# Performance work log

Measured on AMD Instinct MI355X. Metric: run time of the kernel, lower is better.

## Reference

```python
import jax, jax.numpy as jnp
import numpy as np

N_NODES = 30000


def gcn_conv(x, src, dst, ew, W, b, n):
    # x: [N, Fin] -> linear first (PyG GCNConv), then normalized scatter-add
    h = x @ W  # [N, Fout]
    loops = jnp.arange(n, dtype=src.dtype)
    s = jnp.concatenate([src, loops])
    d = jnp.concatenate([dst, loops])
    w = jnp.concatenate([ew, jnp.ones((n,), dtype=ew.dtype)])
    deg = jax.ops.segment_sum(w, d, num_segments=n)
    dinv = jnp.where(deg > 0, jax.lax.rsqrt(jnp.where(deg > 0, deg, 1.0)), 0.0)
    norm = dinv[s] * w * dinv[d]  # [E+N]
    msg = h[s] * norm[:, None]  # [E+N, Fout]
    out = jax.ops.segment_sum(msg, d, num_segments=n)
    return out + b


def setup_inputs() -> dict:
    key = jax.random.key(0)
    ks = jax.random.split(key, 16)
    n, e, f, c = N_NODES, 480000, 64, 64
    dims = [f, 2 * c, 4 * c, 8 * c]  # 64 -> 128 -> 256 -> 512
    num_classes = 40

    def lin(k, fi, fo):
        k1, k2 = jax.random.split(k)
        s = 1.0 / np.sqrt(fi)
        return (jax.random.uniform(k1, (fi, fo), jnp.float32, -s, s),
                jax.random.uniform(k2, (fo,), jnp.float32, -s, s))

    W1, b1 = lin(ks[0], dims[0], dims[1])
    W2, b2 = lin(ks[1], dims[1], dims[2])
    W3, b3 = lin(ks[2], dims[2], dims[3])
    fW1, fb1 = lin(ks[3], dims[3], dims[3])
    fW2, fb2 = lin(ks[4], dims[3], num_classes)
    return {
        "x": jax.random.normal(ks[5], (n, f), jnp.float32),
        "edge_index": jax.random.randint(ks[6], (2, e), 0, n, jnp.int32),
        "edge_attr": jax.random.uniform(ks[7], (e, 1), jnp.float32),
        "W1": W1, "b1": b1, "W2": W2, "b2": b2, "W3": W3, "b3": b3,
        "fW1": fW1, "fb1": fb1, "fW2": fW2, "fb2": fb2,
    }


def reference(x, edge_index, edge_attr, W1, b1, W2, b2, W3, b3, fW1, fb1, fW2, fb2):
    n = x.shape[0]
    src, dst = edge_index[0], edge_index[1]
    ew = edge_attr.squeeze(-1)
    h = jax.nn.relu(gcn_conv(x, src, dst, ew, W1, b1, n))
    h = jax.nn.relu(gcn_conv(h, src, dst, ew, W2, b2, n))
    h = jax.nn.relu(gcn_conv(h, src, dst, ew, W3, b3, n))
    h = jax.nn.relu(h @ fW1 + fb1)
    h = h @ fW2 + fb2
    return jax.nn.log_softmax(h, axis=1)
```

## Files before the change

kernel.cpp:

```cpp
#include <hip/hip_runtime.h>
#include <cstdint>
#include <cstddef>


typedef _Float16 f16;
typedef _Float16 half8 __attribute__((ext_vector_type(8)));
typedef _Float16 half4 __attribute__((ext_vector_type(4)));
typedef float v4f __attribute__((ext_vector_type(4)));
typedef unsigned long long u64;

__device__ inline void gload_lds16(const void* g, void* l) {
    __builtin_amdgcn_global_load_lds(
        (const __attribute__((address_space(1))) unsigned int*)g,
        (__attribute__((address_space(3))) unsigned int*)l, 16, 0, 0);
}


__global__ __launch_bounds__(256) void k_init(u64* packed, int n) {
    int i = blockIdx.x * blockDim.x + threadIdx.x;
    if (i < n) packed[i] = 0ULL;
}

__global__ __launch_bounds__(256) void k_edge1(const int* __restrict__ dst, const float* __restrict__ ew,
                                               u64* __restrict__ packed, int* __restrict__ eslot, int E) {
    int t = blockIdx.x * blockDim.x + threadIdx.x;
    int e0 = t * 4;
    if (e0 + 3 < E) {
        int4 d4 = *(const int4*)(dst + e0);
        float4 w4 = *(const float4*)(ew + e0);
        u64 a0 = ((u64)__float2uint_rn(w4.x * 1048576.f) << 24) | 1ULL;
        u64 a1 = ((u64)__float2uint_rn(w4.y * 1048576.f) << 24) | 1ULL;
        u64 a2 = ((u64)__float2uint_rn(w4.z * 1048576.f) << 24) | 1ULL;
        u64 a3 = ((u64)__float2uint_rn(w4.w * 1048576.f) << 24) | 1ULL;
        u64 o0 = atomicAdd(&packed[d4.x], a0);
        u64 o1 = atomicAdd(&packed[d4.y], a1);
        u64 o2 = atomicAdd(&packed[d4.z], a2);
        u64 o3 = atomicAdd(&packed[d4.w], a3);
        int4 s;
        s.x = (int)(o0 & 0xFFFFFF); s.y = (int)(o1 & 0xFFFFFF);
        s.z = (int)(o2 & 0xFFFFFF); s.w = (int)(o3 & 0xFFFFFF);
        *(int4*)(eslot + e0) = s;
    } else {
        for (int e = e0; e < E; ++e) {
            u64 a = ((u64)__float2uint_rn(ew[e] * 1048576.f) << 24) | 1ULL;
            u64 o = atomicAdd(&packed[dst[e]], a);
            eslot[e] = (int)(o & 0xFFFFFF);
        }
    }
}

__global__ __launch_bounds__(256) void k_dinv_scan1(const u64* __restrict__ packed,
                                                    float* __restrict__ dinv, int* __restrict__ cnt,
                                                    int* __restrict__ bsum, int n) {
    int i = blockIdx.x * 256 + threadIdx.x;
    int c = 0;
    if (i < n) {
        u64 pk = packed[i];
        c = (int)(pk & 0xFFFFFF);
        float d = 1.0f + (float)(pk >> 24) * (1.0f / 1048576.f);
        float r = rsqrtf(d);
        r = r * (1.5f - 0.5f * d * r * r);
        dinv[i] = r;
        cnt[i] = c;
    }
    int v = c;
#pragma unroll
    for (int o = 32; o; o >>= 1) v += __shfl_xor(v, o);
    __shared__ int s[4];
    if ((threadIdx.x & 63) == 0) s[threadIdx.x >> 6] = v;
    __syncthreads();
    if (threadIdx.x == 0) bsum[blockIdx.x] = s[0] + s[1] + s[2] + s[3];
}

__device__ inline int block_scan_incl(int v) {
    __shared__ int ws[4];
    int lane = threadIdx.x & 63, w = threadIdx.x >> 6;
#pragma unroll
    for (int off = 1; off < 64; off <<= 1) {
        int t = __shfl_up(v, off);
        if (lane >= off) v += t;
    }
    if (lane == 63) ws[w] = v;
    __syncthreads();
    int add = 0;
#pragma unroll
    for (int i = 0; i < 4; ++i) add += (i < w) ? ws[i] : 0;
    __syncthreads();
    return v + add;
}

__global__ __launch_bounds__(256) void k_scan2(const int* __restrict__ bsum, int* __restrict__ boff, int nb) {
    __shared__ int carry;
    if (threadIdx.x == 0) carry = 0;
    __syncthreads();
    for (int base = 0; base < nb; base += 256) {
        int i = base + threadIdx.x;
        int v = (i < nb) ? bsum[i] : 0;
        int incl = block_scan_incl(v);
        int c = carry;
        if (i < nb) boff[i] = c + incl - v;
        __syncthreads();
        if (threadIdx.x == 255) carry = c + incl;
        __syncthreads();
    }
}

__global__ __launch_bounds__(256) void k_scan3(const int* __restrict__ cnt, const int* __restrict__ boff,
                                               int* __restrict__ rowptr, int n) {
    int i = blockIdx.x * 256 + threadIdx.x;
    int v = (i < n) ? cnt[i] : 0;
    int incl = block_scan_incl(v);
    if (i < n) rowptr[i] = boff[blockIdx.x] + incl - v;
    if (i == n - 1) rowptr[n] = boff[blockIdx.x] + incl;
}

__global__ __launch_bounds__(256) void k_fill(const int* __restrict__ src, const int* __restrict__ dst,
                                              const float* __restrict__ ew, const int* __restrict__ eslot,
                                              const float* __restrict__ dinv, const int* __restrict__ rowptr,
                                              int* __restrict__ csr_src, float* __restrict__ csr_norm, int E) {
    int e = blockIdx.x * blockDim.x + threadIdx.x;
    if (e < E) {
        int d = dst[e], s = src[e];
        int idx = rowptr[d] + eslot[e];
        csr_src[idx] = s;
        csr_norm[idx] = dinv[s] * ew[e] * dinv[d];
    }
}

struct PrepArgs {
    const float* x; f16* xh; int xt4;
    const float* W[5]; f16* WT[5];
    int lgK[5]; int N[5]; int off[6];
};
__global__ __launch_bounds__(256) void k_prep_cast(PrepArgs a) {
    int i = blockIdx.x * 256 + threadIdx.x;
    if (i < a.xt4) {
        float4 v = *(const float4*)(a.x + (size_t)i * 4);
        half4 h = {(f16)v.x, (f16)v.y, (f16)v.z, (f16)v.w};
        *(half4*)(a.xh + (size_t)i * 4) = h;
        return;
    }
    int w = i - a.xt4;
#pragma unroll
    for (int s = 0; s < 5; ++s) {
        if (w >= a.off[s] && w < a.off[s + 1]) {
            int li = w - a.off[s];
            int K = 1 << a.lgK[s];
            int nr = li >> a.lgK[s], k = li & (K - 1);
            float v = (nr < a.N[s]) ? a.W[s][(size_t)k * a.N[s] + nr] : 0.f;
            a.WT[s][li] = (f16)v;
        }
    }
}

template <int F>
__global__ __launch_bounds__(256) void k_agg(const f16* __restrict__ h,
                                             const float* __restrict__ dinv, const int* __restrict__ rowptr,
                                             const int* __restrict__ csr_src, const float* __restrict__ csr_norm,
                                             f16* __restrict__ o, int n) {
    constexpr int LPN = F / 8;
    constexpr int NPW = 64 / LPN;
    int wave = (int)((blockIdx.x * (unsigned)blockDim.x + threadIdx.x) >> 6);
    int lane = threadIdx.x & 63;
    int grp = lane / LPN, lin = lane % LPN;
    int node = wave * NPW + grp;
    if (node >= n) return;
    float di = dinv[node], w0 = di * di;
    float acc[8];
#pragma unroll
    for (int i = 0; i < 8; ++i) acc[i] = 0.f;

    auto gat = [&](int s, float w) {
        half8 x = *(const half8*)(h + (size_t)s * F + lin * 8);
#pragma unroll
        for (int i = 0; i < 8; ++i) acc[i] += w * (float)x[i];
    };

    gat(node, w0);
    int beg = rowptr[node], end = rowptr[node + 1];
    int j = beg;
    for (; j + 3 < end; j += 4) {
        int s0 = csr_src[j], s1 = csr_src[j + 1], s2 = csr_src[j + 2], s3 = csr_src[j + 3];
        float u0 = csr_norm[j], u1 = csr_norm[j + 1], u2 = csr_norm[j + 2], u3 = csr_norm[j + 3];
        gat(s0, u0); gat(s1, u1); gat(s2, u2); gat(s3, u3);
    }
    for (; j < end; ++j) gat(csr_src[j], csr_norm[j]);

    half8 v;
#pragma unroll
    for (int i = 0; i < 8; ++i) v[i] = (f16)acc[i];
    *(half8*)(o + (size_t)node * F + (size_t)lin * 8) = v;
}

template <int WR, int WC, bool RELU, bool F16OUT>
__global__ __launch_bounds__(256) void k_mm(const f16* __restrict__ A, const f16* __restrict__ BT,
                                            const float* __restrict__ bias,
                                            f16* __restrict__ Ch, float* __restrict__ Cf,
                                            int M, int N, int K, int nB, int nwg) {
    constexpr int TM = WR * 64, TN = WC * 64;
    __shared__ f16 lsA[2][TM * 64];
    __shared__ f16 lsB[2][TN * 64];

    int wg = blockIdx.x;
    int q = nwg >> 3, r = nwg & 7;
    int xcd = wg & 7, lin = wg >> 3;
    int wgs = (xcd < r) ? (xcd * (q + 1) + lin) : (r * (q + 1) + (xcd - r) * q + lin);
    int bm = wgs / nB, bn = wgs % nB;

    int tid = threadIdx.x;
    int lane = tid & 63, wid = tid >> 6;
    int l16 = lane & 15, lhi = lane >> 4;
    int wm = (wid / WC) * 64, wn = (wid % WC) * 64;
    int brow = bm * TM, bcol = bn * TN;

    v4f acc[4][4] = {};

    auto stageA = [&](int buf, int k0) {
#pragma unroll
        for (int it = 0; it < TM / 32; ++it) {
            int b = it * 4096 + tid * 16;
            int row = b >> 7;
            int s = ((b >> 4) & 7) ^ (row & 7);
            gload_lds16(A + (size_t)(brow + row) * K + k0 + s * 8, ((char*)&lsA[buf][0]) + b);
        }
    };
    auto stageB = [&](int buf, int k0) {
#pragma unroll
        for (int it = 0; it < TN / 32; ++it) {
            int b = it * 4096 + tid * 16;
            int row = b >> 7;
            int s = ((b >> 4) & 7) ^ (row & 7);
            gload_lds16(BT + (size_t)(bcol + row) * K + k0 + s * 8, ((char*)&lsB[buf][0]) + b);
        }
    };

    int nk = K >> 6;
    stageA(0, 0);
    stageB(0, 0);
    for (int kt = 0; kt < nk; ++kt) {
        int cur = kt & 1;
        __syncthreads();
        if (kt + 1 < nk) {
            stageA(cur ^ 1, (kt + 1) << 6);
            stageB(cur ^ 1, (kt + 1) << 6);
        }
        half8 bf[2][4];
#pragma unroll
        for (int ks = 0; ks < 2; ++ks)
#pragma unroll
            for (int fn = 0; fn < 4; ++fn) {
                int row = wn + fn * 16 + l16;
                int sidx = (ks * 4 + lhi) ^ (row & 7);
                bf[ks][fn] = *(const half8*)(&lsB[cur][0] + row * 64 + sidx * 8);
            }
#pragma unroll
        for (int ks = 0; ks < 2; ++ks)
#pragma unroll
            for (int fm = 0; fm < 4; ++fm) {
                int row = wm + fm * 16 + l16;
                int sidx = (ks * 4 + lhi) ^ (row & 7);
                half8 af = *(const half8*)(&lsA[cur][0] + row * 64 + sidx * 8);
#pragma unroll
                for (int fn = 0; fn < 4; ++fn)
                    acc[fm][fn] = __builtin_amdgcn_mfma_f32_16x16x32_f16(bf[ks][fn], af, acc[fm][fn], 0, 0, 0);
            }
    }

#pragma unroll
    for (int fm = 0; fm < 4; ++fm) {
        int m = brow + wm + fm * 16 + l16;
        if (m >= M) continue;
#pragma unroll
        for (int fn = 0; fn < 4; ++fn) {
            int nb = bcol + wn + fn * 16 + lhi * 4;
            if (F16OUT) {
                v4f bv = *(const v4f*)(bias + nb);
                v4f v = acc[fm][fn] + bv;
                if (RELU) {
#pragma unroll
                    for (int rr = 0; rr < 4; ++rr) v[rr] = fmaxf(v[rr], 0.f);
                }
                half4 hv = {(f16)v[0], (f16)v[1], (f16)v[2], (f16)v[3]};
                *(half4*)(Ch + (size_t)m * N + nb) = hv;
            } else {
#pragma unroll
                for (int rr = 0; rr < 4; ++rr) {
                    int nn = nb + rr;
                    if (nn < N) {
                        float v = acc[fm][fn][rr] + bias[nn];
                        if (RELU) v = fmaxf(v, 0.f);
                        Cf[(size_t)m * N + nn] = v;
                    }
                }
            }
        }
    }
}


__device__ inline float wred_max(float v) {
#pragma unroll
    for (int o = 32; o; o >>= 1) v = fmaxf(v, __shfl_xor(v, o));
    return v;
}
__device__ inline float wred_sum(float v) {
#pragma unroll
    for (int o = 32; o; o >>= 1) v += __shfl_xor(v, o);
    return v;
}

__global__ __launch_bounds__(256) void k_lsm(const float* __restrict__ in, float* __restrict__ out, int n) {
    int gw = (int)((blockIdx.x * blockDim.x + threadIdx.x) >> 6);
    int lane = threadIdx.x & 63;
    if (gw >= n) return;
    float v = (lane < 40) ? in[(size_t)gw * 40 + lane] : -INFINITY;
    float m = wred_max(v);
    float e = (lane < 40) ? __expf(v - m) : 0.f;
    float s = wred_sum(e);
    if (lane < 40) out[(size_t)gw * 40 + lane] = v - m - __logf(s);
}


extern "C" void kernel_launch(void* const* d_in, const int* in_sizes, int n_in,
                              void* d_out, int out_size, void* d_ws, size_t ws_size,
                              hipStream_t stream) {
    const float* x   = (const float*)d_in[0];
    const int*   ei  = (const int*)d_in[1];
    const float* ea  = (const float*)d_in[2];
    const float* W1  = (const float*)d_in[3];  const float* b1  = (const float*)d_in[4];
    const float* W2  = (const float*)d_in[5];  const float* b2  = (const float*)d_in[6];
    const float* W3  = (const float*)d_in[7];  const float* b3  = (const float*)d_in[8];
    const float* fW1 = (const float*)d_in[9];  const float* fb1 = (const float*)d_in[10];
    const float* fW2 = (const float*)d_in[11]; const float* fb2 = (const float*)d_in[12];

    int n = in_sizes[0] / 64;
    int E = in_sizes[1] / 2;
    int Mpad = ((n + 255) / 256) * 256;
    const int* src = ei;
    const int* dst = ei + E;
    float* out = (float*)d_out;

    char* p = (char*)d_ws;
    auto alloc = [&](size_t bytes) -> char* {
        char* r = p;
        p += (bytes + 255) & ~(size_t)255;
        return r;
    };
    int nb256 = (n + 255) / 256;
    u64*   packed   = (u64*)alloc((size_t)n * 8);
    float* dinv     = (float*)alloc((size_t)n * 4);
    int*   cnt      = (int*)alloc((size_t)n * 4);
    int*   rowptr   = (int*)alloc((size_t)(n + 1) * 4);
    int*   bsum     = (int*)alloc((size_t)nb256 * 4);
    int*   boff     = (int*)alloc((size_t)nb256 * 4);
    int*   eslot    = (int*)alloc((size_t)E * 4);
    int*   csr_src  = (int*)alloc((size_t)E * 4);
    float* csr_norm = (float*)alloc((size_t)E * 4);
    f16* XH  = (f16*)alloc((size_t)Mpad * 64 * 2);
    f16* W1T = (f16*)alloc((size_t)128 * 64 * 2);
    f16* W2T = (f16*)alloc((size_t)256 * 128 * 2);
    f16* W3T = (f16*)alloc((size_t)512 * 256 * 2);
    f16* F1T = (f16*)alloc((size_t)512 * 512 * 2);
    f16* F2T = (f16*)alloc((size_t)128 * 512 * 2);
    f16* AGG = (f16*)alloc((size_t)Mpad * 256 * 2);
    f16* HA  = (f16*)alloc((size_t)Mpad * 512 * 2);
    f16* HB  = (f16*)alloc((size_t)Mpad * 512 * 2);
    float* logits = (float*)alloc((size_t)Mpad * 40 * 4);

    const int tb = 256;
    int nBk = (n + tb - 1) / tb;
    int eB = (E + tb - 1) / tb;
    int e4B = (E / 4 + tb - 1) / tb + 1;
    int waveB = (int)(((size_t)n * 64 + tb - 1) / tb);
    auto aggB = [&](int npw) {
        long waves = (n + npw - 1) / npw;
        return (int)((waves * 64 + tb - 1) / tb);
    };

    k_init<<<nBk, tb, 0, stream>>>(packed, n);
    k_edge1<<<e4B, tb, 0, stream>>>(dst, ea, packed, eslot, E);
    k_dinv_scan1<<<nb256, tb, 0, stream>>>(packed, dinv, cnt, bsum, n);
    k_scan2<<<1, tb, 0, stream>>>(bsum, boff, nb256);
    k_scan3<<<nb256, tb, 0, stream>>>(cnt, boff, rowptr, n);
    k_fill<<<eB, tb, 0, stream>>>(src, dst, ea, eslot, dinv, rowptr, csr_src, csr_norm, E);

    {
        PrepArgs a;
        a.x = x; a.xh = XH; a.xt4 = n * 16;
        a.W[0] = W1;  a.WT[0] = W1T; a.lgK[0] = 6; a.N[0] = 128;
        a.W[1] = W2;  a.WT[1] = W2T; a.lgK[1] = 7; a.N[1] = 256;
        a.W[2] = W3;  a.WT[2] = W3T; a.lgK[2] = 8; a.N[2] = 512;
        a.W[3] = fW1; a.WT[3] = F1T; a.lgK[3] = 9; a.N[3] = 512;
        a.W[4] = fW2; a.WT[4] = F2T; a.lgK[4] = 9; a.N[4] = 40;
        a.off[0] = 0;
        a.off[1] = a.off[0] + 128 * 64;
        a.off[2] = a.off[1] + 256 * 128;
        a.off[3] = a.off[2] + 512 * 256;
        a.off[4] = a.off[3] + 512 * 512;
        a.off[5] = a.off[4] + 128 * 512;
        int tot = a.xt4 + a.off[5];
        k_prep_cast<<<(tot + tb - 1) / tb, tb, 0, stream>>>(a);
    }

    int mB22 = Mpad / 128;
    auto mm22 = [&](const f16* a, const f16* bt, const float* bias, f16* ch, int N, int K) {
        int nB2 = N / 128;
        int nwg = mB22 * nB2;
        k_mm<2, 2, true, true><<<nwg, 256, 0, stream>>>(a, bt, bias, ch, nullptr, n, N, K, nB2, nwg);
    };

    k_agg<64><<<aggB(8), tb, 0, stream>>>(XH, dinv, rowptr, csr_src, csr_norm, AGG, n);
    mm22(AGG, W1T, b1, HA, 128, 64);
    k_agg<128><<<aggB(4), tb, 0, stream>>>(HA, dinv, rowptr, csr_src, csr_norm, AGG, n);
    mm22(AGG, W2T, b2, HB, 256, 128);
    k_agg<256><<<aggB(2), tb, 0, stream>>>(HB, dinv, rowptr, csr_src, csr_norm, AGG, n);
    mm22(AGG, W3T, b3, HA, 512, 256);
    mm22(HA, F1T, fb1, HB, 512, 512);
    {
        int nwg = Mpad / 256;
        k_mm<4, 1, false, false><<<nwg, 256, 0, stream>>>(HB, F2T, fb2, nullptr, logits, n, 40, 512, 1, nwg);
    }
    k_lsm<<<waveB, tb, 0, stream>>>(logits, out, n);
}
```

Baseline: 219.4 us.

## Fuse init into prep, add 256x256 GEMM tiles, fuse final GEMM with log-softmax

The separate zero-init kernel is folded into the prep/cast kernel, which saves one launch. The 128-wide layers (layers 2, 3 and FC1) now run a new 512-thread GEMM with 256x256 tiles, which raises data reuse and cuts the number of workgroups. The last GEMM uses a narrower B tile (64 columns, enough for 40 classes) and computes log-softmax in its epilogue, which removes the logits buffer round-trip and the separate softmax kernel. The bigger tiles use more LDS and registers, so occupancy may drop, and fewer workgroups can leave the GPU underfilled for small layers.

```diff
diff --git a/kernel.cpp b/kernel.cpp
--- a/kernel.cpp
+++ b/kernel.cpp
@@ -15,11 +15,6 @@
         (__attribute__((address_space(3))) unsigned int*)l, 16, 0, 0);
 }
 
-
-__global__ __launch_bounds__(256) void k_init(u64* packed, int n) {
-    int i = blockIdx.x * blockDim.x + threadIdx.x;
-    if (i < n) packed[i] = 0ULL;
-}
 
 __global__ __launch_bounds__(256) void k_edge1(const int* __restrict__ dst, const float* __restrict__ ew,
                                                u64* __restrict__ packed, int* __restrict__ eslot, int E) {
@@ -128,19 +123,22 @@
 }
 
 struct PrepArgs {
+    u64* packed; int n;
     const float* x; f16* xh; int xt4;
     const float* W[5]; f16* WT[5];
     int lgK[5]; int N[5]; int off[6];
 };
-__global__ __launch_bounds__(256) void k_prep_cast(PrepArgs a) {
+__global__ __launch_bounds__(256) void k_prep(PrepArgs a) {
     int i = blockIdx.x * 256 + threadIdx.x;
-    if (i < a.xt4) {
-        float4 v = *(const float4*)(a.x + (size_t)i * 4);
+    if (i < a.n) { a.packed[i] = 0ULL; return; }
+    int j = i - a.n;
+    if (j < a.xt4) {
+        float4 v = *(const float4*)(a.x + (size_t)j * 4);
         half4 h = {(f16)v.x, (f16)v.y, (f16)v.z, (f16)v.w};
-        *(half4*)(a.xh + (size_t)i * 4) = h;
+        *(half4*)(a.xh + (size_t)j * 4) = h;
         return;
     }
-    int w = i - a.xt4;
+    int w = j - a.xt4;
 #pragma unroll
     for (int s = 0; s < 5; ++s) {
         if (w >= a.off[s] && w < a.off[s + 1]) {
@@ -192,15 +190,12 @@
     *(half8*)(o + (size_t)node * F + (size_t)lin * 8) = v;
 }
 
-template <int WR, int WC, bool RELU, bool F16OUT>
+template <bool RELU>
 __global__ __launch_bounds__(256) void k_mm(const f16* __restrict__ A, const f16* __restrict__ BT,
-                                            const float* __restrict__ bias,
-                                            f16* __restrict__ Ch, float* __restrict__ Cf,
+                                            const float* __restrict__ bias, f16* __restrict__ Ch,
                                             int M, int N, int K, int nB, int nwg) {
-    constexpr int TM = WR * 64, TN = WC * 64;
-    __shared__ f16 lsA[2][TM * 64];
-    __shared__ f16 lsB[2][TN * 64];
-
+    __shared__ f16 lsA[2][128 * 64];
+    __shared__ f16 lsB[2][128 * 64];
     int wg = blockIdx.x;
     int q = nwg >> 3, r = nwg & 7;
     int xcd = wg & 7, lin = wg >> 3;
@@ -210,14 +205,14 @@
     int tid = threadIdx.x;
     int lane = tid & 63, wid = tid >> 6;
     int l16 = lane & 15, lhi = lane >> 4;
-    int wm = (wid / WC) * 64, wn = (wid % WC) * 64;
-    int brow = bm * TM, bcol = bn * TN;
+    int wm = (wid >> 1) * 64, wn = (wid & 1) * 64;
+    int brow = bm * 128, bcol = bn * 128;
 
     v4f acc[4][4] = {};
 
     auto stageA = [&](int buf, int k0) {
 #pragma unroll
-        for (int it = 0; it < TM / 32; ++it) {
+        for (int it = 0; it < 4; ++it) {
             int b = it * 4096 + tid * 16;
             int row = b >> 7;
             int s = ((b >> 4) & 7) ^ (row & 7);
@@ -226,7 +221,7 @@
     };
     auto stageB = [&](int buf, int k0) {
 #pragma unroll
-        for (int it = 0; it < TN / 32; ++it) {
+        for (int it = 0; it < 4; ++it) {
             int b = it * 4096 + tid * 16;
             int row = b >> 7;
             int s = ((b >> 4) & 7) ^ (row & 7);
@@ -240,21 +235,16 @@
     for (int kt = 0; kt < nk; ++kt) {
         int cur = kt & 1;
         __syncthreads();
-        if (kt + 1 < nk) {
-            stageA(cur ^ 1, (kt + 1) << 6);
-            stageB(cur ^ 1, (kt + 1) << 6);
-        }
-        half8 bf[2][4];
-#pragma unroll
-        for (int ks = 0; ks < 2; ++ks)
+        if (kt + 1 < nk) { stageA(cur ^ 1, (kt + 1) << 6); stageB(cur ^ 1, (kt + 1) << 6); }
+#pragma unroll
+        for (int ks = 0; ks < 2; ++ks) {
+            half8 bf[4];
 #pragma unroll
             for (int fn = 0; fn < 4; ++fn) {
                 int row = wn + fn * 16 + l16;
                 int sidx = (ks * 4 + lhi) ^ (row & 7);
-                bf[ks][fn] = *(const half8*)(&lsB[cur][0] + row * 64 + sidx * 8);
-            }
-#pragma unroll
-        for (int ks = 0; ks < 2; ++ks)
+                bf[fn] = *(const half8*)(&lsB[cur][0] + row * 64 + sidx * 8);
+            }
 #pragma unroll
             for (int fm = 0; fm < 4; ++fm) {
                 int row = wm + fm * 16 + l16;
@@ -262,10 +252,10 @@
                 half8 af = *(const half8*)(&lsA[cur][0] + row * 64 + sidx * 8);
 #pragma unroll
                 for (int fn = 0; fn < 4; ++fn)
-                    acc[fm][fn] = __builtin_amdgcn_mfma_f32_16x16x32_f16(bf[ks][fn], af, acc[fm][fn], 0, 0, 0);
-            }
-    }
-
+                    acc[fm][fn] = __builtin_amdgcn_mfma_f32_16x16x32_f16(bf[fn], af, acc[fm][fn], 0, 0, 0);
+            }
+        }
+    }
 #pragma unroll
     for (int fm = 0; fm < 4; ++fm) {
         int m = brow + wm + fm * 16 + l16;
@@ -273,51 +263,209 @@
 #pragma unroll
         for (int fn = 0; fn < 4; ++fn) {
             int nb = bcol + wn + fn * 16 + lhi * 4;
-            if (F16OUT) {
-                v4f bv = *(const v4f*)(bias + nb);
-                v4f v = acc[fm][fn] + bv;
-                if (RELU) {
-#pragma unroll
-                    for (int rr = 0; rr < 4; ++rr) v[rr] = fmaxf(v[rr], 0.f);
+            v4f bv = *(const v4f*)(bias + nb);
+            v4f v = acc[fm][fn] + bv;
+            if (RELU) {
+#pragma unroll
+                for (int rr = 0; rr < 4; ++rr) v[rr] = fmaxf(v[rr], 0.f);
+            }
+            half4 hv = {(f16)v[0], (f16)v[1], (f16)v[2], (f16)v[3]};
+            *(half4*)(Ch + (size_t)m * N + nb) = hv;
+        }
+    }
+}
+
+template <bool RELU>
+__global__ __launch_bounds__(512, 2) void k_mm8(const f16* __restrict__ A, const f16* __restrict__ BT,
+                                                const float* __restrict__ bias, f16* __restrict__ Ch,
+                                                int M, int N, int K, int nB, int nwg) {
+    __shared__ f16 lsA[2][256 * 64];
+    __shared__ f16 lsB[2][256 * 64];
+    int wg = blockIdx.x;
+    int q = nwg >> 3, r = nwg & 7;
+    int xcd = wg & 7, lin = wg >> 3;
+    int wgs = (xcd < r) ? (xcd * (q + 1) + lin) : (r * (q + 1) + (xcd - r) * q + lin);
+    int bm = wgs / nB, bn = wgs % nB;
+
+    int tid = threadIdx.x;
+    int lane = tid & 63, wid = tid >> 6;
+    int l16 = lane & 15, lhi = lane >> 4;
+    int wm = (wid >> 2) * 128, wn = (wid & 3) * 64;
+    int brow = bm * 256, bcol = bn * 256;
+
+    v4f acc[8][4] = {};
+
+    auto stageA = [&](int buf, int k0) {
+#pragma unroll
+        for (int it = 0; it < 4; ++it) {
+            int b = it * 8192 + tid * 16;
+            int row = b >> 7;
+            int s = ((b >> 4) & 7) ^ (row & 7);
+            gload_lds16(A + (size_t)(brow + row) * K + k0 + s * 8, ((char*)&lsA[buf][0]) + b);
+        }
+    };
+    auto stageB = [&](int buf, int k0) {
+#pragma unroll
+        for (int it = 0; it < 4; ++it) {
+            int b = it * 8192 + tid * 16;
+            int row = b >> 7;
+            int s = ((b >> 4) & 7) ^ (row & 7);
+            gload_lds16(BT + (size_t)(bcol + row) * K + k0 + s * 8, ((char*)&lsB[buf][0]) + b);
+        }
+    };
+
+    int nk = K >> 6;
+    stageA(0, 0);
+    stageB(0, 0);
+    for (int kt = 0; kt < nk; ++kt) {
+        int cur = kt & 1;
+        __syncthreads();
+        if (kt + 1 < nk) { stageA(cur ^ 1, (kt + 1) << 6); stageB(cur ^ 1, (kt + 1) << 6); }
+#pragma unroll
+        for (int ks = 0; ks < 2; ++ks) {
+            half8 bf[4];
+#pragma unroll
+            for (int fn = 0; fn < 4; ++fn) {
+                int row = wn + fn * 16 + l16;
+                int sidx = (ks * 4 + lhi) ^ (row & 7);
+                bf[fn] = *(const half8*)(&lsB[cur][0] + row * 64 + sidx * 8);
+            }
+#pragma unroll
+            for (int fm = 0; fm < 8; ++fm) {
+                int row = wm + fm * 16 + l16;
+                int sidx = (ks * 4 + lhi) ^ (row & 7);
+                half8 af = *(const half8*)(&lsA[cur][0] + row * 64 + sidx * 8);
+#pragma unroll
+                for (int fn = 0; fn < 4; ++fn)
+                    acc[fm][fn] = __builtin_amdgcn_mfma_f32_16x16x32_f16(bf[fn], af, acc[fm][fn], 0, 0, 0);
+            }
+        }
+    }
+#pragma unroll
+    for (int fm = 0; fm < 8; ++fm) {
+        int m = brow + wm + fm * 16 + l16;
+        if (m >= M) continue;
+#pragma unroll
+        for (int fn = 0; fn < 4; ++fn) {
+            int nb = bcol + wn + fn * 16 + lhi * 4;
+            v4f bv = *(const v4f*)(bias + nb);
+            v4f v = acc[fm][fn] + bv;
+            if (RELU) {
+#pragma unroll
+                for (int rr = 0; rr < 4; ++rr) v[rr] = fmaxf(v[rr], 0.f);
+            }
+            half4 hv = {(f16)v[0], (f16)v[1], (f16)v[2], (f16)v[3]};
+            *(half4*)(Ch + (size_t)m * N + nb) = hv;
+        }
+    }
+}
+
+__global__ __launch_bounds__(256) void k_mmfc2(const f16* __restrict__ A, const f16* __restrict__ BT,
+                                               const float* __restrict__ bias, float* __restrict__ out,
+                                               int M, int K) {
+    __shared__ f16 lsA[2][256 * 64];
+    __shared__ f16 lsB[2][64 * 64];
+    int bm = blockIdx.x;
+    int tid = threadIdx.x;
+    int lane = tid & 63, wid = tid >> 6;
+    int l16 = lane & 15, lhi = lane >> 4;
+    int wm = wid * 64;
+    int brow = bm * 256;
+
+    v4f acc[4][4] = {};
+
+    auto stageA = [&](int buf, int k0) {
+#pragma unroll
+        for (int it = 0; it < 8; ++it) {
+            int b = it * 4096 + tid * 16;
+            int row = b >> 7;
+            int s = ((b >> 4) & 7) ^ (row & 7);
+            gload_lds16(A + (size_t)(brow + row) * K + k0 + s * 8, ((char*)&lsA[buf][0]) + b);
+        }
+    };
+    auto stageB = [&](int buf, int k0) {
+#pragma unroll
+        for (int it = 0; it < 2; ++it) {
+            int b = it * 4096 + tid * 16;
+            int row = b >> 7;
+            int s = ((b >> 4) & 7) ^ (row & 7);
+            gload_lds16(BT + (size_t)row * K + k0 + s * 8, ((char*)&lsB[buf][0]) + b);
+        }
+    };
+
+    int nk = K >> 6;
+    stageA(0, 0);
+    stageB(0, 0);
+    for (int kt = 0; kt < nk; ++kt) {
+        int cur = kt & 1;
+        __syncthreads();
+        if (kt + 1 < nk) { stageA(cur ^ 1, (kt + 1) << 6); stageB(cur ^ 1, (kt + 1) << 6); }
+#pragma unroll
+        for (int ks = 0; ks < 2; ++ks) {
+            half8 bf[4];
+#pragma unroll
+            for (int fn = 0; fn < 4; ++fn) {
+                int row = fn * 16 + l16;
+                int sidx = (ks * 4 + lhi) ^ (row & 7);
+                bf[fn] = *(const half8*)(&lsB[cur][0] + row * 64 + sidx * 8);
+            }
+#pragma unroll
+            for (int fm = 0; fm < 4; ++fm) {
+                int row = wm + fm * 16 + l16;
+                int sidx = (ks * 4 + lhi) ^ (row & 7);
+                half8 af = *(const half8*)(&lsA[cur][0] + row * 64 + sidx * 8);
+#pragma unroll
+                for (int fn = 0; fn < 4; ++fn)
+                    acc[fm][fn] = __builtin_amdgcn_mfma_f32_16x16x32_f16(bf[fn], af, acc[fm][fn], 0, 0, 0);
+            }
+        }
+    }
+
+    float bv[4][4];
+#pragma unroll
+    for (int fn = 0; fn < 4; ++fn)
+#pragma unroll
+        for (int rr = 0; rr < 4; ++rr) {
+            int nn = fn * 16 + lhi * 4 + rr;
+            bv[fn][rr] = (nn < 40) ? bias[nn] : 0.f;
+        }
+
+#pragma unroll
+    for (int fm = 0; fm < 4; ++fm) {
+        int m = brow + wm + fm * 16 + l16;
+        float v[4][4];
+        float mx = -INFINITY;
+#pragma unroll
+        for (int fn = 0; fn < 4; ++fn)
+#pragma unroll
+            for (int rr = 0; rr < 4; ++rr) {
+                int nn = fn * 16 + lhi * 4 + rr;
+                v[fn][rr] = acc[fm][fn][rr] + bv[fn][rr];
+                if (nn < 40) mx = fmaxf(mx, v[fn][rr]);
+            }
+        mx = fmaxf(mx, __shfl_xor(mx, 16));
+        mx = fmaxf(mx, __shfl_xor(mx, 32));
+        float s = 0.f;
+#pragma unroll
+        for (int fn = 0; fn < 3; ++fn)
+#pragma unroll
+            for (int rr = 0; rr < 4; ++rr) {
+                int nn = fn * 16 + lhi * 4 + rr;
+                if (nn < 40) s += __expf(v[fn][rr] - mx);
+            }
+        s += __shfl_xor(s, 16);
+        s += __shfl_xor(s, 32);
+        float ls = __logf(s);
+        if (m < M) {
+#pragma unroll
+            for (int fn = 0; fn < 3; ++fn)
+#pragma unroll
+                for (int rr = 0; rr < 4; ++rr) {
+                    int nn = fn * 16 + lhi * 4 + rr;
+                    if (nn < 40) out[(size_t)m * 40 + nn] = v[fn][rr] - mx - ls;
                 }
-                half4 hv = {(f16)v[0], (f16)v[1], (f16)v[2], (f16)v[3]};
-                *(half4*)(Ch + (size_t)m * N + nb) = hv;
-            } else {
-#pragma unroll
-                for (int rr = 0; rr < 4; ++rr) {
-                    int nn = nb + rr;
-                    if (nn < N) {
-                        float v = acc[fm][fn][rr] + bias[nn];
-                        if (RELU) v = fmaxf(v, 0.f);
-                        Cf[(size_t)m * N + nn] = v;
-                    }
-                }
-            }
-        }
-    }
-}
-
-
-__device__ inline float wred_max(float v) {
-#pragma unroll
-    for (int o = 32; o; o >>= 1) v = fmaxf(v, __shfl_xor(v, o));
-    return v;
-}
-__device__ inline float wred_sum(float v) {
-#pragma unroll
-    for (int o = 32; o; o >>= 1) v += __shfl_xor(v, o);
-    return v;
-}
-
-__global__ __launch_bounds__(256) void k_lsm(const float* __restrict__ in, float* __restrict__ out, int n) {
-    int gw = (int)((blockIdx.x * blockDim.x + threadIdx.x) >> 6);
-    int lane = threadIdx.x & 63;
-    if (gw >= n) return;
-    float v = (lane < 40) ? in[(size_t)gw * 40 + lane] : -INFINITY;
-    float m = wred_max(v);
-    float e = (lane < 40) ? __expf(v - m) : 0.f;
-    float s = wred_sum(e);
-    if (lane < 40) out[(size_t)gw * 40 + lane] = v - m - __logf(s);
+        }
+    }
 }
 
 
@@ -361,31 +509,22 @@
     f16* W2T = (f16*)alloc((size_t)256 * 128 * 2);
     f16* W3T = (f16*)alloc((size_t)512 * 256 * 2);
     f16* F1T = (f16*)alloc((size_t)512 * 512 * 2);
-    f16* F2T = (f16*)alloc((size_t)128 * 512 * 2);
+    f16* F2T = (f16*)alloc((size_t)64 * 512 * 2);
     f16* AGG = (f16*)alloc((size_t)Mpad * 256 * 2);
     f16* HA  = (f16*)alloc((size_t)Mpad * 512 * 2);
     f16* HB  = (f16*)alloc((size_t)Mpad * 512 * 2);
-    float* logits = (float*)alloc((size_t)Mpad * 40 * 4);
 
     const int tb = 256;
-    int nBk = (n + tb - 1) / tb;
     int eB = (E + tb - 1) / tb;
     int e4B = (E / 4 + tb - 1) / tb + 1;
-    int waveB = (int)(((size_t)n * 64 + tb - 1) / tb);
     auto aggB = [&](int npw) {
         long waves = (n + npw - 1) / npw;
         return (int)((waves * 64 + tb - 1) / tb);
     };
 
-    k_init<<<nBk, tb, 0, stream>>>(packed, n);
-    k_edge1<<<e4B, tb, 0, stream>>>(dst, ea, packed, eslot, E);
-    k_dinv_scan1<<<nb256, tb, 0, stream>>>(packed, dinv, cnt, bsum, n);
-    k_scan2<<<1, tb, 0, stream>>>(bsum, boff, nb256);
-    k_scan3<<<nb256, tb, 0, stream>>>(cnt, boff, rowptr, n);
-    k_fill<<<eB, tb, 0, stream>>>(src, dst, ea, eslot, dinv, rowptr, csr_src, csr_norm, E);
-
     {
         PrepArgs a;
+        a.packed = packed; a.n = n;
         a.x = x; a.xh = XH; a.xt4 = n * 16;
         a.W[0] = W1;  a.WT[0] = W1T; a.lgK[0] = 6; a.N[0] = 128;
         a.W[1] = W2;  a.WT[1] = W2T; a.lgK[1] = 7; a.N[1] = 256;
@@ -397,28 +536,32 @@
         a.off[2] = a.off[1] + 256 * 128;
         a.off[3] = a.off[2] + 512 * 256;
         a.off[4] = a.off[3] + 512 * 512;
-        a.off[5] = a.off[4] + 128 * 512;
-        int tot = a.xt4 + a.off[5];
-        k_prep_cast<<<(tot + tb - 1) / tb, tb, 0, stream>>>(a);
-    }
-
-    int mB22 = Mpad / 128;
-    auto mm22 = [&](const f16* a, const f16* bt, const float* bias, f16* ch, int N, int K) {
-        int nB2 = N / 128;
-        int nwg = mB22 * nB2;
-        k_mm<2, 2, true, true><<<nwg, 256, 0, stream>>>(a, bt, bias, ch, nullptr, n, N, K, nB2, nwg);
+        a.off[5] = a.off[4] + 64 * 512;
+        int tot = a.n + a.xt4 + a.off[5];
+        k_prep<<<(tot + tb - 1) / tb, tb, 0, stream>>>(a);
+    }
+
+    k_edge1<<<e4B, tb, 0, stream>>>(dst, ea, packed, eslot, E);
+    k_dinv_scan1<<<nb256, tb, 0, stream>>>(packed, dinv, cnt, bsum, n);
+    k_scan2<<<1, tb, 0, stream>>>(bsum, boff, nb256);
+    k_scan3<<<nb256, tb, 0, stream>>>(cnt, boff, rowptr, n);
+    k_fill<<<eB, tb, 0, stream>>>(src, dst, ea, eslot, dinv, rowptr, csr_src, csr_norm, E);
+
+    auto mm8 = [&](const f16* a, const f16* bt, const float* bias, f16* ch, int N, int K) {
+        int nB2 = N / 256;
+        int nwg = (Mpad / 256) * nB2;
+        k_mm8<true><<<nwg, 512, 0, stream>>>(a, bt, bias, ch, n, N, K, nB2, nwg);
     };
 
     k_agg<64><<<aggB(8), tb, 0, stream>>>(XH, dinv, rowptr, csr_src, csr_norm, AGG, n);
-    mm22(AGG, W1T, b1, HA, 128, 64);
+    {
+        int nwg = Mpad / 128;
+        k_mm<true><<<nwg, 256, 0, stream>>>(AGG, W1T, b1, HA, n, 128, 64, 1, nwg);
+    }
     k_agg<128><<<aggB(4), tb, 0, stream>>>(HA, dinv, rowptr, csr_src, csr_norm, AGG, n);
-    mm22(AGG, W2T, b2, HB, 256, 128);
+    mm8(AGG, W2T, b2, HB, 256, 128);
     k_agg<256><<<aggB(2), tb, 0, stream>>>(HB, dinv, rowptr, csr_src, csr_norm, AGG, n);
-    mm22(AGG, W3T, b3, HA, 512, 256);
-    mm22(HA, F1T, fb1, HB, 512, 512);
-    {
-        int nwg = Mpad / 256;
-        k_mm<4, 1, false, false><<<nwg, 256, 0, stream>>>(HB, F2T, fb2, nullptr, logits, n, 40, 512, 1, nwg);
-    }
-    k_lsm<<<waveB, tb, 0, stream>>>(logits, out, n);
-}
+    mm8(AGG, W3T, b3, HA, 512, 256);
+    mm8(HA, F1T, fb1, HB, 512, 512);
+    k_mmfc2<<<Mpad / 256, 256, 0, stream>>>(HB, F2T, fb2, out, n, 512);
+}
```

New measurement: 206.0 us. 1.07x faster.
